# Performance work log

Hardware: AMD Instinct MI355X
Metric: run time of the kernel (lower is better)

## Reference

```python
import jax, jax.numpy as jnp
import numpy as np

HEADS = 8
WS = 8


def setup_inputs() -> dict:
    key = jax.random.key(0)
    k1, k2, k3, k4 = jax.random.split(key, 4)
    C = 256
    x = jax.random.normal(k1, (4, C, 256, 256), dtype=jnp.float32)
    w_qkv = jax.random.normal(k2, (3 * C, C), dtype=jnp.float32) * (C ** -0.5)
    w_out = jax.random.normal(k3, (C, C), dtype=jnp.float32) * (C ** -0.5)
    b_out = jax.random.normal(k4, (C,), dtype=jnp.float32) * 0.02
    return {"x": x, "w_qkv": w_qkv, "w_out": w_out, "b_out": b_out}


def reference(x, w_qkv, w_out, b_out):
    B, C, H, W = x.shape
    ws, heads = WS, HEADS
    d = C // heads
    scale = d ** -0.5
    pad_h = (ws - H % ws) % ws
    pad_w = (ws - W % ws) % ws
    xp = jnp.pad(x, ((0, 0), (0, 0), (0, pad_h), (0, pad_w)))
    Hp, Wp = H + pad_h, W + pad_w
    nh, nw = Hp // ws, Wp // ws
    # b c (nh wh) (nw ww) -> (b nh nw) c wh ww
    xw = xp.reshape(B, C, nh, ws, nw, ws).transpose(0, 2, 4, 1, 3, 5)
    xw = xw.reshape(B * nh * nw, C, ws, ws)
    # 1x1 conv qkv projection (bias-free): [3C,C] x [Bw,C,h,w]
    qkv = jnp.einsum('oc,bchw->bohw', w_qkv, xw)
    q, k, v = jnp.split(qkv, 3, axis=1)

    def to_heads(t):
        # b (h d) x y -> b h (x y) d
        Bw = t.shape[0]
        return t.reshape(Bw, heads, d, ws * ws).transpose(0, 1, 3, 2)

    q, k, v = to_heads(q), to_heads(k), to_heads(v)
    attn = jnp.einsum('bhid,bhjd->bhij', q, k) * scale
    attn = jax.nn.softmax(attn, axis=-1)
    out = jnp.einsum('bhij,bhjd->bhid', attn, v)
    # b h (x y) d -> b (h d) x y
    Bw = out.shape[0]
    out = out.transpose(0, 1, 3, 2).reshape(Bw, C, ws, ws)
    out = jnp.einsum('oc,bchw->bohw', w_out, out) + b_out[None, :, None, None]
    # (b nh nw) c wh ww -> b c (nh wh) (nw ww)
    out = out.reshape(B, nh, nw, C, ws, ws).transpose(0, 3, 1, 4, 2, 5)
    out = out.reshape(B, C, Hp, Wp)
    return out[:, :, :H, :W]
```

## Files before the change

### kernel.cpp

```cpp
#include <hip/hip_runtime.h>

typedef __attribute__((ext_vector_type(4))) float f32x4;
typedef __attribute__((ext_vector_type(8))) short bf16x8;
typedef __attribute__((ext_vector_type(4))) unsigned int u32x4;

#define MFMA32 __builtin_amdgcn_mfma_f32_16x16x32_bf16

__device__ __forceinline__ unsigned short f2bf(float f) {
  unsigned int u = __float_as_uint(f);
  return (unsigned short)((u + 0x7FFFu + ((u >> 16) & 1u)) >> 16);
}
__device__ __forceinline__ unsigned int pack2(float a, float b) {
  return __builtin_amdgcn_perm(__float_as_uint(b) + 0x8000u,
                               __float_as_uint(a) + 0x8000u, 0x07060302u);
}
__device__ __forceinline__ bf16x8 mk8(unsigned int a, unsigned int b,
                                      unsigned int c, unsigned int d) {
  u32x4 u = {a, b, c, d};
  return __builtin_bit_cast(bf16x8, u);
}
__device__ __forceinline__ int xsw(int tok, int cb) {
  return (tok * 512 + cb) ^ ((((tok >> 3) ^ tok) & 7) << 4);
}

__global__ void convw_kernel(const float* __restrict__ wqkv,
                             const float* __restrict__ wout,
                             unsigned short* __restrict__ dst) {
  int i = blockIdx.x * 256 + threadIdx.x;
  if (i < 196608) dst[i] = f2bf(wqkv[i]);
  if (i < 65536) dst[196608 + i] = f2bf(wout[i]);
}

__global__ __launch_bounds__(256, 2) void wattn_kernel(
    const float* __restrict__ x, const unsigned short* __restrict__ wqkv,
    const unsigned short* __restrict__ wout, const float* __restrict__ bo,
    float* __restrict__ y) {
  __shared__ __align__(16) char lds[32768];

  const int tid = threadIdx.x;
  const int l = tid & 63;
  const int w = tid >> 6;
  const int lo = l & 15;
  const int dg = l >> 4;

  const int bid = blockIdx.x;
  const int rw = ((bid & 7) << 9) | (bid >> 3);
  const int b = rw >> 10;
  const int rem = rw & 1023;
  const int wy = rem >> 5;
  const int wx = rem & 31;

  const size_t wbase = ((size_t)b * 65536 + (size_t)wy * 8) * 256 + (size_t)wx * 8;
  const float* xw = x + wbase;
  float* yw = y + wbase;

  {
    const int irow = lo >> 1;
    const int jq = lo & 1;
    const float* xp = xw + irow * 256 + jq * 4;
    const int tok0 = irow * 8 + jq * 4;
#pragma unroll 2
    for (int cc = 0; cc < 4; ++cc) {
      const int cb = w * 64 + cc * 16 + dg * 4;
      f32x4 v0 = *(const f32x4*)(xp + (size_t)(cb + 0) * 65536);
      f32x4 v1 = *(const f32x4*)(xp + (size_t)(cb + 1) * 65536);
      f32x4 v2 = *(const f32x4*)(xp + (size_t)(cb + 2) * 65536);
      f32x4 v3 = *(const f32x4*)(xp + (size_t)(cb + 3) * 65536);
#pragma unroll
      for (int t = 0; t < 4; ++t) {
        uint2 uu;
        uu.x = pack2(v0[t], v1[t]);
        uu.y = pack2(v2[t], v3[t]);
        *(uint2*)(lds + xsw(tok0 + t, cb * 2)) = uu;
      }
    }
  }
  __syncthreads();

  const float lscale = 0.17677669529663687f * 1.4426950408889634f;

  unsigned int outp[2][2][4][2];

#pragma unroll 1
  for (int hh = 0; hh < 2; ++hh) {
    const int h = w * 2 + hh;
    const unsigned short* wp = wqkv + (size_t)(h * 32 + lo) * 256 + dg * 8;

    bf16x8 qf[4], kf[4];
    {
      f32x4 qa[2][4];
#pragma unroll
      for (int a = 0; a < 2; ++a)
#pragma unroll
        for (int it = 0; it < 4; ++it) qa[a][it] = {0.f, 0.f, 0.f, 0.f};
#pragma unroll 2
      for (int kk = 0; kk < 8; ++kk) {
        bf16x8 xf[4];
#pragma unroll
        for (int it = 0; it < 4; ++it)
          xf[it] = *(const bf16x8*)(lds + xsw(it * 16 + lo, kk * 64 + dg * 16));
        bf16x8 wq0 = *(const bf16x8*)(wp + kk * 32);
        bf16x8 wq1 = *(const bf16x8*)(wp + 4096 + kk * 32);
#pragma unroll
        for (int it = 0; it < 4; ++it) {
          qa[0][it] = MFMA32(wq0, xf[it], qa[0][it], 0, 0, 0);
          qa[1][it] = MFMA32(wq1, xf[it], qa[1][it], 0, 0, 0);
        }
      }
#pragma unroll
      for (int it = 0; it < 4; ++it)
        qf[it] = mk8(pack2(qa[0][it][0], qa[0][it][1]), pack2(qa[0][it][2], qa[0][it][3]),
                     pack2(qa[1][it][0], qa[1][it][1]), pack2(qa[1][it][2], qa[1][it][3]));
    }
    {
      f32x4 ka[2][4];
#pragma unroll
      for (int a = 0; a < 2; ++a)
#pragma unroll
        for (int it = 0; it < 4; ++it) ka[a][it] = {0.f, 0.f, 0.f, 0.f};
#pragma unroll 2
      for (int kk = 0; kk < 8; ++kk) {
        bf16x8 xf[4];
#pragma unroll
        for (int it = 0; it < 4; ++it)
          xf[it] = *(const bf16x8*)(lds + xsw(it * 16 + lo, kk * 64 + dg * 16));
        bf16x8 wk0 = *(const bf16x8*)(wp + 65536 + kk * 32);
        bf16x8 wk1 = *(const bf16x8*)(wp + 69632 + kk * 32);
#pragma unroll
        for (int it = 0; it < 4; ++it) {
          ka[0][it] = MFMA32(wk0, xf[it], ka[0][it], 0, 0, 0);
          ka[1][it] = MFMA32(wk1, xf[it], ka[1][it], 0, 0, 0);
        }
      }
#pragma unroll
      for (int it = 0; it < 4; ++it)
        kf[it] = mk8(pack2(ka[0][it][0], ka[0][it][1]), pack2(ka[0][it][2], ka[0][it][3]),
                     pack2(ka[1][it][0], ka[1][it][1]), pack2(ka[1][it][2], ka[1][it][3]));
    }
    bf16x8 vf[2][2];
    {
      f32x4 va[4][2];
#pragma unroll
      for (int tb = 0; tb < 4; ++tb)
#pragma unroll
        for (int dt = 0; dt < 2; ++dt) va[tb][dt] = {0.f, 0.f, 0.f, 0.f};
#pragma unroll 2
      for (int kk = 0; kk < 8; ++kk) {
        bf16x8 xf[4];
#pragma unroll
        for (int tb = 0; tb < 4; ++tb)
          xf[tb] = *(const bf16x8*)(lds + xsw(tb * 16 + lo, kk * 64 + dg * 16));
        bf16x8 wv0 = *(const bf16x8*)(wp + 131072 + kk * 32);
        bf16x8 wv1 = *(const bf16x8*)(wp + 135168 + kk * 32);
#pragma unroll
        for (int tb = 0; tb < 4; ++tb) {
          va[tb][0] = MFMA32(xf[tb], wv0, va[tb][0], 0, 0, 0);
          va[tb][1] = MFMA32(xf[tb], wv1, va[tb][1], 0, 0, 0);
        }
      }
#pragma unroll
      for (int sb = 0; sb < 2; ++sb)
#pragma unroll
        for (int dt = 0; dt < 2; ++dt)
          vf[sb][dt] = mk8(pack2(va[2 * sb][dt][0], va[2 * sb][dt][1]),
                           pack2(va[2 * sb][dt][2], va[2 * sb][dt][3]),
                           pack2(va[2 * sb + 1][dt][0], va[2 * sb + 1][dt][1]),
                           pack2(va[2 * sb + 1][dt][2], va[2 * sb + 1][dt][3]));
    }

#pragma unroll
    for (int it = 0; it < 4; ++it) {
      f32x4 stt[4];
#pragma unroll
      for (int jt = 0; jt < 4; ++jt) {
        f32x4 z = {0.f, 0.f, 0.f, 0.f};
        stt[jt] = MFMA32(kf[jt], qf[it], z, 0, 0, 0);
      }
      float s = 0.f;
#pragma unroll
      for (int jt = 0; jt < 4; ++jt)
#pragma unroll
        for (int t = 0; t < 4; ++t) {
          float e = exp2f(stt[jt][t] * lscale);
          stt[jt][t] = e;
          s += e;
        }
      s += __shfl_xor(s, 16, 64);
      s += __shfl_xor(s, 32, 64);
      const float rs = 1.0f / s;

      bf16x8 pp0 = mk8(pack2(stt[0][0], stt[0][1]), pack2(stt[0][2], stt[0][3]),
                       pack2(stt[1][0], stt[1][1]), pack2(stt[1][2], stt[1][3]));
      bf16x8 pp1 = mk8(pack2(stt[2][0], stt[2][1]), pack2(stt[2][2], stt[2][3]),
                       pack2(stt[3][0], stt[3][1]), pack2(stt[3][2], stt[3][3]));
#pragma unroll
      for (int dt = 0; dt < 2; ++dt) {
        f32x4 z = {0.f, 0.f, 0.f, 0.f};
        f32x4 o = MFMA32(vf[0][dt], pp0, z, 0, 0, 0);
        o = MFMA32(vf[1][dt], pp1, o, 0, 0, 0);
        o *= rs;
        outp[hh][dt][it][0] = pack2(o[0], o[1]);
        outp[hh][dt][it][1] = pack2(o[2], o[3]);
      }
    }
  }

  __syncthreads();

#pragma unroll
  for (int hh = 0; hh < 2; ++hh) {
    const int h = w * 2 + hh;
#pragma unroll
    for (int dt = 0; dt < 2; ++dt)
#pragma unroll
      for (int it = 0; it < 4; ++it) {
        uint2 uu;
        uu.x = outp[hh][dt][it][0];
        uu.y = outp[hh][dt][it][1];
        *(uint2*)(lds + xsw(it * 16 + lo, h * 64 + dt * 32 + dg * 8)) = uu;
      }
  }
  __syncthreads();

#pragma unroll 1
  for (int oh = 0; oh < 2; ++oh) {
    const unsigned short* wo0 =
        wout + (size_t)(w * 64 + oh * 32 + lo) * 256 + dg * 8;
    f32x4 ya[2][4];
#pragma unroll
    for (int ot = 0; ot < 2; ++ot)
#pragma unroll
      for (int it = 0; it < 4; ++it) ya[ot][it] = {0.f, 0.f, 0.f, 0.f};
#pragma unroll 2
    for (int kk = 0; kk < 8; ++kk) {
      bf16x8 bt[4];
#pragma unroll
      for (int it = 0; it < 4; ++it)
        bt[it] = *(const bf16x8*)(lds + xsw(it * 16 + lo, kk * 64 + dg * 16));
      bf16x8 wf0 = *(const bf16x8*)(wo0 + kk * 32);
      bf16x8 wf1 = *(const bf16x8*)(wo0 + 4096 + kk * 32);
#pragma unroll
      for (int it = 0; it < 4; ++it) {
        ya[0][it] = MFMA32(bt[it], wf0, ya[0][it], 0, 0, 0);
        ya[1][it] = MFMA32(bt[it], wf1, ya[1][it], 0, 0, 0);
      }
    }
#pragma unroll
    for (int ot = 0; ot < 2; ++ot) {
      const int orow = w * 64 + oh * 32 + ot * 16 + lo;
      const float bv = bo[orow];
#pragma unroll
      for (int it = 0; it < 4; ++it) {
        f32x4 r = ya[ot][it];
        r[0] += bv; r[1] += bv; r[2] += bv; r[3] += bv;
        const int tok0 = it * 16 + dg * 4;
        *(f32x4*)(yw + (size_t)orow * 65536 +
                  (size_t)(tok0 >> 3) * 256 + (tok0 & 7)) = r;
      }
    }
  }
}

extern "C" void kernel_launch(void* const* d_in, const int* in_sizes, int n_in,
                              void* d_out, int out_size, void* d_ws, size_t ws_size,
                              hipStream_t stream) {
  const float* x = (const float*)d_in[0];
  const float* wqkv = (const float*)d_in[1];
  const float* wout = (const float*)d_in[2];
  const float* bo = (const float*)d_in[3];
  float* y = (float*)d_out;
  unsigned short* wbf = (unsigned short*)d_ws;

  convw_kernel<<<768, 256, 0, stream>>>(wqkv, wout, wbf);
  wattn_kernel<<<4096, 256, 0, stream>>>(x, wbf, wbf + 196608, bo, y);
}
```

Before: 398.3 us.

## Process two horizontally adjacent windows per block to reuse weights and widen stores

Each block now handles two neighbouring 8x8 windows. Both are staged into a doubled 64KB LDS buffer, and attention runs for each window in turn. The output projection loads each w_out fragment once and applies it to both windows, and the two results go out as adjacent 16-float row segments. This halves the grid, cuts repeated weight fetches for the output projection, and improves write coalescing. In exchange, doubled LDS per block may lower occupancy to fewer resident blocks per CU.

```diff
diff --git a/kernel.cpp b/kernel.cpp
--- a/kernel.cpp
+++ b/kernel.cpp
@@ -35,7 +35,7 @@
     const float* __restrict__ x, const unsigned short* __restrict__ wqkv,
     const unsigned short* __restrict__ wout, const float* __restrict__ bo,
     float* __restrict__ y) {
-  __shared__ __align__(16) char lds[32768];
+  __shared__ __align__(16) char lds[65536];
 
   const int tid = threadIdx.x;
   const int l = tid & 63;
@@ -44,20 +44,22 @@
   const int dg = l >> 4;
 
   const int bid = blockIdx.x;
-  const int rw = ((bid & 7) << 9) | (bid >> 3);
-  const int b = rw >> 10;
-  const int rem = rw & 1023;
-  const int wy = rem >> 5;
-  const int wx = rem & 31;
-
-  const size_t wbase = ((size_t)b * 65536 + (size_t)wy * 8) * 256 + (size_t)wx * 8;
+  const int rw = ((bid & 7) << 8) | (bid >> 3);
+  const int b = rw >> 9;
+  const int rem = rw & 511;
+  const int wy = rem >> 4;
+  const int wxp = rem & 15;
+
+  const size_t wbase = (size_t)b * 16777216 + (size_t)wy * 2048 + (size_t)wxp * 16;
   const float* xw = x + wbase;
   float* yw = y + wbase;
 
-  {
+#pragma unroll 1
+  for (int wsel = 0; wsel < 2; ++wsel) {
+    char* XSb = lds + wsel * 32768;
     const int irow = lo >> 1;
     const int jq = lo & 1;
-    const float* xp = xw + irow * 256 + jq * 4;
+    const float* xp = xw + wsel * 8 + irow * 256 + jq * 4;
     const int tok0 = irow * 8 + jq * 4;
 #pragma unroll 2
     for (int cc = 0; cc < 4; ++cc) {
@@ -71,7 +73,7 @@
         uint2 uu;
         uu.x = pack2(v0[t], v1[t]);
         uu.y = pack2(v2[t], v3[t]);
-        *(uint2*)(lds + xsw(tok0 + t, cb * 2)) = uu;
+        *(uint2*)(XSb + xsw(tok0 + t, cb * 2)) = uu;
       }
     }
   }
@@ -79,184 +81,187 @@
 
   const float lscale = 0.17677669529663687f * 1.4426950408889634f;
 
-  unsigned int outp[2][2][4][2];
-
 #pragma unroll 1
-  for (int hh = 0; hh < 2; ++hh) {
-    const int h = w * 2 + hh;
-    const unsigned short* wp = wqkv + (size_t)(h * 32 + lo) * 256 + dg * 8;
-
-    bf16x8 qf[4], kf[4];
-    {
-      f32x4 qa[2][4];
-#pragma unroll
-      for (int a = 0; a < 2; ++a)
-#pragma unroll
-        for (int it = 0; it < 4; ++it) qa[a][it] = {0.f, 0.f, 0.f, 0.f};
-#pragma unroll 2
-      for (int kk = 0; kk < 8; ++kk) {
-        bf16x8 xf[4];
+  for (int wsel = 0; wsel < 2; ++wsel) {
+    char* XSb = lds + wsel * 32768;
+    unsigned int outp[2][2][4][2];
+
+#pragma unroll
+    for (int hh = 0; hh < 2; ++hh) {
+      const int h = w * 2 + hh;
+      const unsigned short* wp = wqkv + (size_t)(h * 32 + lo) * 256 + dg * 8;
+
+      bf16x8 qf[4], kf[4];
+      {
+        f32x4 qa[2][4];
+#pragma unroll
+        for (int a = 0; a < 2; ++a)
+#pragma unroll
+          for (int it = 0; it < 4; ++it) qa[a][it] = {0.f, 0.f, 0.f, 0.f};
+#pragma unroll 2
+        for (int kk = 0; kk < 8; ++kk) {
+          bf16x8 xf[4];
+#pragma unroll
+          for (int it = 0; it < 4; ++it)
+            xf[it] = *(const bf16x8*)(XSb + xsw(it * 16 + lo, kk * 64 + dg * 16));
+          bf16x8 wq0 = *(const bf16x8*)(wp + kk * 32);
+          bf16x8 wq1 = *(const bf16x8*)(wp + 4096 + kk * 32);
+#pragma unroll
+          for (int it = 0; it < 4; ++it) {
+            qa[0][it] = MFMA32(wq0, xf[it], qa[0][it], 0, 0, 0);
+            qa[1][it] = MFMA32(wq1, xf[it], qa[1][it], 0, 0, 0);
+          }
+        }
 #pragma unroll
         for (int it = 0; it < 4; ++it)
-          xf[it] = *(const bf16x8*)(lds + xsw(it * 16 + lo, kk * 64 + dg * 16));
-        bf16x8 wq0 = *(const bf16x8*)(wp + kk * 32);
-        bf16x8 wq1 = *(const bf16x8*)(wp + 4096 + kk * 32);
+          qf[it] = mk8(pack2(qa[0][it][0], qa[0][it][1]), pack2(qa[0][it][2], qa[0][it][3]),
+                       pack2(qa[1][it][0], qa[1][it][1]), pack2(qa[1][it][2], qa[1][it][3]));
+      }
+      {
+        f32x4 ka[2][4];
+#pragma unroll
+        for (int a = 0; a < 2; ++a)
+#pragma unroll
+          for (int it = 0; it < 4; ++it) ka[a][it] = {0.f, 0.f, 0.f, 0.f};
+#pragma unroll 2
+        for (int kk = 0; kk < 8; ++kk) {
+          bf16x8 xf[4];
+#pragma unroll
+          for (int it = 0; it < 4; ++it)
+            xf[it] = *(const bf16x8*)(XSb + xsw(it * 16 + lo, kk * 64 + dg * 16));
+          bf16x8 wk0 = *(const bf16x8*)(wp + 65536 + kk * 32);
+          bf16x8 wk1 = *(const bf16x8*)(wp + 69632 + kk * 32);
+#pragma unroll
+          for (int it = 0; it < 4; ++it) {
+            ka[0][it] = MFMA32(wk0, xf[it], ka[0][it], 0, 0, 0);
+            ka[1][it] = MFMA32(wk1, xf[it], ka[1][it], 0, 0, 0);
+          }
+        }
+#pragma unroll
+        for (int it = 0; it < 4; ++it)
+          kf[it] = mk8(pack2(ka[0][it][0], ka[0][it][1]), pack2(ka[0][it][2], ka[0][it][3]),
+                       pack2(ka[1][it][0], ka[1][it][1]), pack2(ka[1][it][2], ka[1][it][3]));
+      }
+      bf16x8 vf[2][2];
+      {
+        f32x4 va[4][2];
+#pragma unroll
+        for (int tb = 0; tb < 4; ++tb)
+#pragma unroll
+          for (int dt = 0; dt < 2; ++dt) va[tb][dt] = {0.f, 0.f, 0.f, 0.f};
+#pragma unroll 2
+        for (int kk = 0; kk < 8; ++kk) {
+          bf16x8 xf[4];
+#pragma unroll
+          for (int tb = 0; tb < 4; ++tb)
+            xf[tb] = *(const bf16x8*)(XSb + xsw(tb * 16 + lo, kk * 64 + dg * 16));
+          bf16x8 wv0 = *(const bf16x8*)(wp + 131072 + kk * 32);
+          bf16x8 wv1 = *(const bf16x8*)(wp + 135168 + kk * 32);
+#pragma unroll
+          for (int tb = 0; tb < 4; ++tb) {
+            va[tb][0] = MFMA32(xf[tb], wv0, va[tb][0], 0, 0, 0);
+            va[tb][1] = MFMA32(xf[tb], wv1, va[tb][1], 0, 0, 0);
+          }
+        }
+#pragma unroll
+        for (int sb = 0; sb < 2; ++sb)
+#pragma unroll
+          for (int dt = 0; dt < 2; ++dt)
+            vf[sb][dt] = mk8(pack2(va[2 * sb][dt][0], va[2 * sb][dt][1]),
+                             pack2(va[2 * sb][dt][2], va[2 * sb][dt][3]),
+                             pack2(va[2 * sb + 1][dt][0], va[2 * sb + 1][dt][1]),
+                             pack2(va[2 * sb + 1][dt][2], va[2 * sb + 1][dt][3]));
+      }
+
+#pragma unroll
+      for (int it = 0; it < 4; ++it) {
+        f32x4 stt[4];
+#pragma unroll
+        for (int jt = 0; jt < 4; ++jt) {
+          f32x4 z = {0.f, 0.f, 0.f, 0.f};
+          stt[jt] = MFMA32(kf[jt], qf[it], z, 0, 0, 0);
+        }
+        float s = 0.f;
+#pragma unroll
+        for (int jt = 0; jt < 4; ++jt)
+#pragma unroll
+          for (int t = 0; t < 4; ++t) {
+            float e = exp2f(stt[jt][t] * lscale);
+            stt[jt][t] = e;
+            s += e;
+          }
+        s += __shfl_xor(s, 16, 64);
+        s += __shfl_xor(s, 32, 64);
+        const float rs = 1.0f / s;
+
+        bf16x8 pp0 = mk8(pack2(stt[0][0], stt[0][1]), pack2(stt[0][2], stt[0][3]),
+                         pack2(stt[1][0], stt[1][1]), pack2(stt[1][2], stt[1][3]));
+        bf16x8 pp1 = mk8(pack2(stt[2][0], stt[2][1]), pack2(stt[2][2], stt[2][3]),
+                         pack2(stt[3][0], stt[3][1]), pack2(stt[3][2], stt[3][3]));
+#pragma unroll
+        for (int dt = 0; dt < 2; ++dt) {
+          f32x4 z = {0.f, 0.f, 0.f, 0.f};
+          f32x4 o = MFMA32(vf[0][dt], pp0, z, 0, 0, 0);
+          o = MFMA32(vf[1][dt], pp1, o, 0, 0, 0);
+          o *= rs;
+          outp[hh][dt][it][0] = pack2(o[0], o[1]);
+          outp[hh][dt][it][1] = pack2(o[2], o[3]);
+        }
+      }
+    }
+
+    __syncthreads();
+
+#pragma unroll
+    for (int hh = 0; hh < 2; ++hh) {
+      const int h = w * 2 + hh;
+#pragma unroll
+      for (int dt = 0; dt < 2; ++dt)
 #pragma unroll
         for (int it = 0; it < 4; ++it) {
-          qa[0][it] = MFMA32(wq0, xf[it], qa[0][it], 0, 0, 0);
-          qa[1][it] = MFMA32(wq1, xf[it], qa[1][it], 0, 0, 0);
-        }
-      }
-#pragma unroll
-      for (int it = 0; it < 4; ++it)
-        qf[it] = mk8(pack2(qa[0][it][0], qa[0][it][1]), pack2(qa[0][it][2], qa[0][it][3]),
-                     pack2(qa[1][it][0], qa[1][it][1]), pack2(qa[1][it][2], qa[1][it][3]));
-    }
-    {
-      f32x4 ka[2][4];
-#pragma unroll
-      for (int a = 0; a < 2; ++a)
-#pragma unroll
-        for (int it = 0; it < 4; ++it) ka[a][it] = {0.f, 0.f, 0.f, 0.f};
-#pragma unroll 2
-      for (int kk = 0; kk < 8; ++kk) {
-        bf16x8 xf[4];
-#pragma unroll
-        for (int it = 0; it < 4; ++it)
-          xf[it] = *(const bf16x8*)(lds + xsw(it * 16 + lo, kk * 64 + dg * 16));
-        bf16x8 wk0 = *(const bf16x8*)(wp + 65536 + kk * 32);
-        bf16x8 wk1 = *(const bf16x8*)(wp + 69632 + kk * 32);
-#pragma unroll
-        for (int it = 0; it < 4; ++it) {
-          ka[0][it] = MFMA32(wk0, xf[it], ka[0][it], 0, 0, 0);
-          ka[1][it] = MFMA32(wk1, xf[it], ka[1][it], 0, 0, 0);
-        }
-      }
-#pragma unroll
-      for (int it = 0; it < 4; ++it)
-        kf[it] = mk8(pack2(ka[0][it][0], ka[0][it][1]), pack2(ka[0][it][2], ka[0][it][3]),
-                     pack2(ka[1][it][0], ka[1][it][1]), pack2(ka[1][it][2], ka[1][it][3]));
-    }
-    bf16x8 vf[2][2];
-    {
-      f32x4 va[4][2];
-#pragma unroll
-      for (int tb = 0; tb < 4; ++tb)
-#pragma unroll
-        for (int dt = 0; dt < 2; ++dt) va[tb][dt] = {0.f, 0.f, 0.f, 0.f};
-#pragma unroll 2
-      for (int kk = 0; kk < 8; ++kk) {
-        bf16x8 xf[4];
-#pragma unroll
-        for (int tb = 0; tb < 4; ++tb)
-          xf[tb] = *(const bf16x8*)(lds + xsw(tb * 16 + lo, kk * 64 + dg * 16));
-        bf16x8 wv0 = *(const bf16x8*)(wp + 131072 + kk * 32);
-        bf16x8 wv1 = *(const bf16x8*)(wp + 135168 + kk * 32);
-#pragma unroll
-        for (int tb = 0; tb < 4; ++tb) {
-          va[tb][0] = MFMA32(xf[tb], wv0, va[tb][0], 0, 0, 0);
-          va[tb][1] = MFMA32(xf[tb], wv1, va[tb][1], 0, 0, 0);
-        }
-      }
-#pragma unroll
-      for (int sb = 0; sb < 2; ++sb)
-#pragma unroll
-        for (int dt = 0; dt < 2; ++dt)
-          vf[sb][dt] = mk8(pack2(va[2 * sb][dt][0], va[2 * sb][dt][1]),
-                           pack2(va[2 * sb][dt][2], va[2 * sb][dt][3]),
-                           pack2(va[2 * sb + 1][dt][0], va[2 * sb + 1][dt][1]),
-                           pack2(va[2 * sb + 1][dt][2], va[2 * sb + 1][dt][3]));
-    }
-
-#pragma unroll
-    for (int it = 0; it < 4; ++it) {
-      f32x4 stt[4];
-#pragma unroll
-      for (int jt = 0; jt < 4; ++jt) {
-        f32x4 z = {0.f, 0.f, 0.f, 0.f};
-        stt[jt] = MFMA32(kf[jt], qf[it], z, 0, 0, 0);
-      }
-      float s = 0.f;
-#pragma unroll
-      for (int jt = 0; jt < 4; ++jt)
-#pragma unroll
-        for (int t = 0; t < 4; ++t) {
-          float e = exp2f(stt[jt][t] * lscale);
-          stt[jt][t] = e;
-          s += e;
-        }
-      s += __shfl_xor(s, 16, 64);
-      s += __shfl_xor(s, 32, 64);
-      const float rs = 1.0f / s;
-
-      bf16x8 pp0 = mk8(pack2(stt[0][0], stt[0][1]), pack2(stt[0][2], stt[0][3]),
-                       pack2(stt[1][0], stt[1][1]), pack2(stt[1][2], stt[1][3]));
-      bf16x8 pp1 = mk8(pack2(stt[2][0], stt[2][1]), pack2(stt[2][2], stt[2][3]),
-                       pack2(stt[3][0], stt[3][1]), pack2(stt[3][2], stt[3][3]));
-#pragma unroll
-      for (int dt = 0; dt < 2; ++dt) {
-        f32x4 z = {0.f, 0.f, 0.f, 0.f};
-        f32x4 o = MFMA32(vf[0][dt], pp0, z, 0, 0, 0);
-        o = MFMA32(vf[1][dt], pp1, o, 0, 0, 0);
-        o *= rs;
-        outp[hh][dt][it][0] = pack2(o[0], o[1]);
-        outp[hh][dt][it][1] = pack2(o[2], o[3]);
-      }
-    }
-  }
-
-  __syncthreads();
-
-#pragma unroll
-  for (int hh = 0; hh < 2; ++hh) {
-    const int h = w * 2 + hh;
-#pragma unroll
-    for (int dt = 0; dt < 2; ++dt)
-#pragma unroll
-      for (int it = 0; it < 4; ++it) {
-        uint2 uu;
-        uu.x = outp[hh][dt][it][0];
-        uu.y = outp[hh][dt][it][1];
-        *(uint2*)(lds + xsw(it * 16 + lo, h * 64 + dt * 32 + dg * 8)) = uu;
-      }
+          uint2 uu;
+          uu.x = outp[hh][dt][it][0];
+          uu.y = outp[hh][dt][it][1];
+          *(uint2*)(XSb + xsw(it * 16 + lo, h * 64 + dt * 32 + dg * 8)) = uu;
+        }
+    }
   }
   __syncthreads();
 
 #pragma unroll 1
-  for (int oh = 0; oh < 2; ++oh) {
+  for (int oq = 0; oq < 4; ++oq) {
     const unsigned short* wo0 =
-        wout + (size_t)(w * 64 + oh * 32 + lo) * 256 + dg * 8;
-    f32x4 ya[2][4];
-#pragma unroll
-    for (int ot = 0; ot < 2; ++ot)
-#pragma unroll
-      for (int it = 0; it < 4; ++it) ya[ot][it] = {0.f, 0.f, 0.f, 0.f};
+        wout + (size_t)(w * 64 + oq * 16 + lo) * 256 + dg * 8;
+    f32x4 ya0[4], ya1[4];
+#pragma unroll
+    for (int it = 0; it < 4; ++it) {
+      ya0[it] = {0.f, 0.f, 0.f, 0.f};
+      ya1[it] = {0.f, 0.f, 0.f, 0.f};
+    }
 #pragma unroll 2
     for (int kk = 0; kk < 8; ++kk) {
-      bf16x8 bt[4];
-#pragma unroll
-      for (int it = 0; it < 4; ++it)
-        bt[it] = *(const bf16x8*)(lds + xsw(it * 16 + lo, kk * 64 + dg * 16));
-      bf16x8 wf0 = *(const bf16x8*)(wo0 + kk * 32);
-      bf16x8 wf1 = *(const bf16x8*)(wo0 + 4096 + kk * 32);
+      bf16x8 wf = *(const bf16x8*)(wo0 + kk * 32);
 #pragma unroll
       for (int it = 0; it < 4; ++it) {
-        ya[0][it] = MFMA32(bt[it], wf0, ya[0][it], 0, 0, 0);
-        ya[1][it] = MFMA32(bt[it], wf1, ya[1][it], 0, 0, 0);
-      }
-    }
-#pragma unroll
-    for (int ot = 0; ot < 2; ++ot) {
-      const int orow = w * 64 + oh * 32 + ot * 16 + lo;
-      const float bv = bo[orow];
-#pragma unroll
-      for (int it = 0; it < 4; ++it) {
-        f32x4 r = ya[ot][it];
-        r[0] += bv; r[1] += bv; r[2] += bv; r[3] += bv;
-        const int tok0 = it * 16 + dg * 4;
-        *(f32x4*)(yw + (size_t)orow * 65536 +
-                  (size_t)(tok0 >> 3) * 256 + (tok0 & 7)) = r;
-      }
+        bf16x8 b0 = *(const bf16x8*)(lds + xsw(it * 16 + lo, kk * 64 + dg * 16));
+        bf16x8 b1 = *(const bf16x8*)(lds + 32768 + xsw(it * 16 + lo, kk * 64 + dg * 16));
+        ya0[it] = MFMA32(b0, wf, ya0[it], 0, 0, 0);
+        ya1[it] = MFMA32(b1, wf, ya1[it], 0, 0, 0);
+      }
+    }
+    const int orow = w * 64 + oq * 16 + lo;
+    const float bv = bo[orow];
+#pragma unroll
+    for (int it = 0; it < 4; ++it) {
+      f32x4 r0 = ya0[it];
+      f32x4 r1 = ya1[it];
+      r0[0] += bv; r0[1] += bv; r0[2] += bv; r0[3] += bv;
+      r1[0] += bv; r1[1] += bv; r1[2] += bv; r1[3] += bv;
+      const int tok0 = it * 16 + dg * 4;
+      float* dst = yw + (size_t)orow * 65536 +
+                   (size_t)(tok0 >> 3) * 256 + (tok0 & 7);
+      *(f32x4*)dst = r0;
+      *(f32x4*)(dst + 8) = r1;
     }
   }
 }
@@ -272,5 +277,5 @@
   unsigned short* wbf = (unsigned short*)d_ws;
 
   convw_kernel<<<768, 256, 0, stream>>>(wqkv, wout, wbf);
-  wattn_kernel<<<4096, 256, 0, stream>>>(x, wbf, wbf + 196608, bo, y);
-}
+  wattn_kernel<<<2048, 256, 0, stream>>>(x, wbf, wbf + 196608, bo, y);
+}
```

After: 356.0 us. -10.6%, faster.
